# Performance work log

Measured on AMD Instinct MI355X. Metric: run time of the kernel, lower is better.

## Reference

```python
import jax, jax.numpy as jnp
import numpy as np

N_NODES = 100000
N_EDGES = 1600000
IN_DIM = 128
HID = 128
OUT = 64


def gcn_conv(x, src, dst, W, b, n_nodes):
    # x: [N, Din] -> [N, Dout]; symmetric-normalized GCN with self-loops (PyG GCNConv defaults)
    h = x @ W  # transform first (as PyG does)
    loop = jnp.arange(n_nodes, dtype=src.dtype)
    s = jnp.concatenate([src, loop])
    d = jnp.concatenate([dst, loop])
    deg = jax.ops.segment_sum(jnp.ones_like(d, dtype=h.dtype), d, num_segments=n_nodes)
    dis = jnp.where(deg > 0, jax.lax.rsqrt(deg), 0.0)
    norm = dis[s] * dis[d]  # [E+N]
    msgs = h[s] * norm[:, None]  # gather-transform
    out = jax.ops.segment_sum(msgs, d, num_segments=n_nodes)  # scatter-add
    return out + b


def setup_inputs() -> dict:
    key = jax.random.key(0)
    ks = jax.random.split(key, 12)
    x = jax.random.normal(ks[0], (N_NODES, IN_DIM), dtype=jnp.float32)
    edge_index = jax.random.randint(ks[1], (2, N_EDGES), 0, N_NODES, dtype=jnp.int32)
    def lin(k, fan_in, fan_out):
        bound = 1.0 / np.sqrt(fan_in)
        kw, kb = jax.random.split(k)
        W = jax.random.uniform(kw, (fan_in, fan_out), minval=-bound, maxval=bound, dtype=jnp.float32)
        b = jax.random.uniform(kb, (fan_out,), minval=-bound, maxval=bound, dtype=jnp.float32)
        return W, b
    W1, b1 = lin(ks[2], IN_DIM, HID)
    W2, b2 = lin(ks[3], HID, HID)
    Wp1, bp1 = lin(ks[4], HID, HID)
    Wp2, bp2 = lin(ks[5], HID, OUT)
    return {"x": x, "edge_index": edge_index,
            "W1": W1, "b1": b1, "W2": W2, "b2": b2,
            "Wp1": Wp1, "bp1": bp1, "Wp2": Wp2, "bp2": bp2}


def reference(x, edge_index, W1, b1, W2, b2, Wp1, bp1, Wp2, bp2):
    n = x.shape[0]
    src, dst = edge_index[0], edge_index[1]
    # layer 1: GCNConv + relu (dropout inactive at eval)
    h = jax.nn.relu(gcn_conv(x, src, dst, W1, b1, n))
    # layer 2
    h = jax.nn.relu(gcn_conv(h, src, dst, W2, b2, n))
    # post MLP head
    h = h @ Wp1 + bp1
    h = h @ Wp2 + bp2
    return jax.nn.log_softmax(h, axis=1)
```

## Files before the change

### kernel.cpp

```cpp
#include <hip/hip_runtime.h>
#include <hip/hip_bf16.h>
#include <cstdint>

typedef __attribute__((ext_vector_type(8))) short short8;
typedef __attribute__((ext_vector_type(16))) float f32x16;
typedef unsigned short us;

#define BIN_SHIFT 9
#define BIN_NODES 512
#define CAPB 12288
#define EPB 4096

__device__ __forceinline__ float bflo(uint32_t u) { return __builtin_bit_cast(float, u << 16); }
__device__ __forceinline__ float bfhi(uint32_t u) { return __builtin_bit_cast(float, u & 0xffff0000u); }

__device__ __forceinline__ us f32_to_bf16_rne(float f) {
  uint32_t u = __builtin_bit_cast(uint32_t, f);
  u += 0x7fffu + ((u >> 16) & 1u);
  return (us)(u >> 16);
}

__device__ __forceinline__ void split2(float f, us& h, us& l) {
  uint32_t u = __builtin_bit_cast(uint32_t, f);
  h = (us)(u >> 16);
  float fh = __builtin_bit_cast(float, u & 0xffff0000u);
  float r = f - fh;
  l = (us)(__builtin_bit_cast(uint32_t, r) >> 16);
}

__global__ void k_prep(const float* __restrict__ W1, const float* __restrict__ W2,
                       const float* __restrict__ Wp1, const float* __restrict__ Wp2,
                       const float* __restrict__ bp1, const float* __restrict__ bp2,
                       us* __restrict__ Wt1h, us* __restrict__ Wt1l,
                       us* __restrict__ Wt2h, us* __restrict__ Wt2l,
                       us* __restrict__ Wch, us* __restrict__ Wcl, float* __restrict__ bc,
                       int* __restrict__ gcur, int* __restrict__ hzero) {
  int blk = blockIdx.x, tid = threadIdx.x;
  if (blk < 128) {
    const float* W = (blk < 64) ? W1 : W2;
    us* Wh = (blk < 64) ? Wt1h : Wt2h;
    us* Wl = (blk < 64) ? Wt1l : Wt2l;
    int idx = (blk & 63) * 256 + tid;
    int k = idx >> 7, n = idx & 127;
    us h, l;
    split2(W[idx], h, l);
    Wh[n * 128 + k] = h;
    Wl[n * 128 + k] = l;
  } else if (blk < 160) {
    int idx = (blk - 128) * 256 + tid;
    int k = idx >> 6, j = idx & 63;
    float acc = 0.f;
    for (int t = 0; t < 128; ++t) acc += Wp1[k * 128 + t] * Wp2[t * 64 + j];
    us h, l;
    split2(acc, h, l);
    Wch[j * 128 + k] = h;
    Wcl[j * 128 + k] = l;
  } else {
    gcur[tid] = 0;
    if (tid < 64) {
      hzero[tid] = 0;
      float acc = bp2[tid];
      for (int t = 0; t < 128; ++t) acc += bp1[t] * Wp2[t * 64 + tid];
      bc[tid] = acc;
    }
  }
}

__global__ __launch_bounds__(256) void k_binA(
    const int* __restrict__ src, const int* __restrict__ dst,
    uint2* __restrict__ binbuf, int* __restrict__ gcur, int E, int nbins) {
  __shared__ uint2 stage[EPB];
  __shared__ int cnt[256], base[256], cur[256], gbase[256];
  int tid = threadIdx.x;
  int e0 = blockIdx.x * EPB;
  int ne = min(EPB, E - e0);
  if (ne <= 0) return;
  cnt[tid] = 0;
  __syncthreads();
  for (int i = tid; i < ne; i += 256) atomicAdd(&cnt[dst[e0 + i] >> BIN_SHIFT], 1);
  __syncthreads();
  if (tid < 64) {
    int carry = 0;
#pragma unroll
    for (int c = 0; c < 4; ++c) {
      int v = cnt[c * 64 + tid];
      int incl = v;
#pragma unroll
      for (int off = 1; off < 64; off <<= 1) {
        int t = __shfl_up(incl, off, 64);
        if (tid >= off) incl += t;
      }
      base[c * 64 + tid] = carry + incl - v;
      carry += __shfl(incl, 63, 64);
    }
  }
  __syncthreads();
  if (tid < nbins && cnt[tid] > 0) gbase[tid] = atomicAdd(&gcur[tid], cnt[tid]);
  cur[tid] = base[tid];
  __syncthreads();
  for (int i = tid; i < ne; i += 256) {
    int d = dst[e0 + i], s = src[e0 + i];
    int p = atomicAdd(&cur[d >> BIN_SHIFT], 1);
    stage[p] = make_uint2((unsigned)d, (unsigned)s);
  }
  __syncthreads();
  for (int i = tid; i < ne; i += 256) {
    uint2 en = stage[i];
    int b = en.x >> BIN_SHIFT;
    int gi = gbase[b] + (i - base[b]);
    if (gi < CAPB) binbuf[(size_t)b * CAPB + gi] = en;
  }
}

__global__ __launch_bounds__(256) void k_passB(
    const uint2* __restrict__ binbuf, const int* __restrict__ gcur,
    int* __restrict__ deg, float* __restrict__ dis, int* __restrict__ start,
    int* __restrict__ col, int N, int nbins) {
  __shared__ int hist[512], lstart[512], cur[512];
  __shared__ int colstage[CAPB];
  __shared__ int binbase_s;
  int b = blockIdx.x, tid = threadIdx.x;
  int node0 = b << BIN_SHIFT;
  int cnt = min(gcur[b], CAPB);
  hist[tid] = 0; hist[tid + 256] = 0;
  __syncthreads();
  const uint2* bp = binbuf + (size_t)b * CAPB;
  for (int i = tid; i < cnt; i += 256) atomicAdd(&hist[bp[i].x & (BIN_NODES - 1)], 1);
  __syncthreads();
  if (tid < 64) {
    int s = 0;
    for (int i = tid; i < b; i += 64) s += min(gcur[i], CAPB);
#pragma unroll
    for (int off = 32; off; off >>= 1) s += __shfl_xor(s, off, 64);
    if (tid == 0) binbase_s = s;
    int carry = 0;
#pragma unroll
    for (int c = 0; c < 8; ++c) {
      int v = hist[c * 64 + tid];
      int incl = v;
#pragma unroll
      for (int off = 1; off < 64; off <<= 1) {
        int t = __shfl_up(incl, off, 64);
        if (tid >= off) incl += t;
      }
      lstart[c * 64 + tid] = carry + incl - v;
      carry += __shfl(incl, 63, 64);
    }
  }
  __syncthreads();
  int binbase = binbase_s;
  for (int i = tid; i < 512; i += 256) {
    int node = node0 + i;
    if (node < N) {
      int dg = hist[i];
      deg[node] = dg;
      dis[node] = rsqrtf((float)(dg + 1));
      start[node] = binbase + lstart[i];
    }
  }
  cur[tid] = lstart[tid]; cur[tid + 256] = lstart[tid + 256];
  __syncthreads();
  for (int i = tid; i < cnt; i += 256) {
    uint2 en = bp[i];
    int p = atomicAdd(&cur[en.x & (BIN_NODES - 1)], 1);
    colstage[p] = (int)en.y;
  }
  __syncthreads();
  for (int i = tid; i < cnt; i += 256) col[binbase + i] = colstage[i];
}

__global__ __launch_bounds__(256) void k_gemm1(
    const float* __restrict__ A, const us* __restrict__ Wh,
    const us* __restrict__ Wl, const float* __restrict__ dis,
    us* __restrict__ out_bf16, int N, int ntiles) {
  __shared__ us As[32 * 136];
  int tid = threadIdx.x;
  int wave = tid >> 6, lane = tid & 63;
  int n0 = wave * 32;
  int nn = n0 + (lane & 31);
  int khalf = (lane >> 5) * 8;
  int m = lane & 31;

  short8 bh[8], bl[8];
#pragma unroll
  for (int c = 0; c < 8; ++c) {
    bh[c] = *(const short8*)&Wh[nn * 128 + c * 16 + khalf];
    bl[c] = *(const short8*)&Wl[nn * 128 + c * 16 + khalf];
  }

  for (int t = blockIdx.x; t < ntiles; t += gridDim.x) {
    int row0 = t * 32;
    __syncthreads();
    for (int j = tid; j < 1024; j += 256) {
      int r = j >> 5, c = j & 31;
      int row = row0 + r;
      float4 v = make_float4(0.f, 0.f, 0.f, 0.f);
      if (row < N) v = *(const float4*)&A[(size_t)row * 128 + c * 4];
      *(ushort4*)&As[r * 136 + c * 4] = make_ushort4(
          f32_to_bf16_rne(v.x), f32_to_bf16_rne(v.y),
          f32_to_bf16_rne(v.z), f32_to_bf16_rne(v.w));
    }
    __syncthreads();

    f32x16 acc = {};
#pragma unroll
    for (int c = 0; c < 8; ++c) {
      short8 ah = *(const short8*)&As[m * 136 + c * 16 + khalf];
      acc = __builtin_amdgcn_mfma_f32_32x32x16_bf16(ah, bh[c], acc, 0, 0, 0);
      acc = __builtin_amdgcn_mfma_f32_32x32x16_bf16(ah, bl[c], acc, 0, 0, 0);
    }

    int col = n0 + (lane & 31);
    int rbase = row0 + 4 * (lane >> 5);
#pragma unroll
    for (int reg = 0; reg < 16; ++reg) {
      int row = rbase + (reg & 3) + 8 * (reg >> 2);
      if (row < N) {
        float v = acc[reg] * dis[row];
        out_bf16[(size_t)row * 128 + col] = f32_to_bf16_rne(v);
      }
    }
  }
}

__global__ __launch_bounds__(256) void k_gemm2(
    const us* __restrict__ A, const us* __restrict__ Wh,
    const us* __restrict__ Wl, const float* __restrict__ dis,
    us* __restrict__ out_bf16, int N, int ntiles) {
  __shared__ us As[32 * 136];
  int tid = threadIdx.x;
  int wave = tid >> 6, lane = tid & 63;
  int n0 = wave * 32;
  int nn = n0 + (lane & 31);
  int khalf = (lane >> 5) * 8;
  int m = lane & 31;

  short8 bh[8], bl[8];
#pragma unroll
  for (int c = 0; c < 8; ++c) {
    bh[c] = *(const short8*)&Wh[nn * 128 + c * 16 + khalf];
    bl[c] = *(const short8*)&Wl[nn * 128 + c * 16 + khalf];
  }

  for (int t = blockIdx.x; t < ntiles; t += gridDim.x) {
    int row0 = t * 32;
    __syncthreads();
    for (int j = tid; j < 512; j += 256) {
      int r = j >> 4, c = j & 15;
      int row = row0 + r;
      uint4 v = make_uint4(0u, 0u, 0u, 0u);
      if (row < N) v = *(const uint4*)&A[(size_t)row * 128 + c * 8];
      *(uint4*)&As[r * 136 + c * 8] = v;
    }
    __syncthreads();

    f32x16 acc = {};
#pragma unroll
    for (int c = 0; c < 8; ++c) {
      short8 ah = *(const short8*)&As[m * 136 + c * 16 + khalf];
      acc = __builtin_amdgcn_mfma_f32_32x32x16_bf16(ah, bh[c], acc, 0, 0, 0);
      acc = __builtin_amdgcn_mfma_f32_32x32x16_bf16(ah, bl[c], acc, 0, 0, 0);
    }

    int col = n0 + (lane & 31);
    int rbase = row0 + 4 * (lane >> 5);
#pragma unroll
    for (int reg = 0; reg < 16; ++reg) {
      int row = rbase + (reg & 3) + 8 * (reg >> 2);
      if (row < N) {
        float v = acc[reg] * dis[row];
        out_bf16[(size_t)row * 128 + col] = f32_to_bf16_rne(v);
      }
    }
  }
}

__global__ __launch_bounds__(512) void k_gather(
    const us* __restrict__ h, us* __restrict__ o,
    const int* __restrict__ start, const int* __restrict__ deg,
    const int* __restrict__ col, const float* __restrict__ dis,
    const float* __restrict__ bias, int N) {
  int wave = threadIdx.x >> 6, lane = threadIdx.x & 63;
  int node = blockIdx.x * 8 + wave;
  if (node >= N) return;
  const uint32_t* h1 = (const uint32_t*)h;
  uint32_t u = h1[(size_t)node * 64 + lane];
  float a0 = bflo(u), b0 = bfhi(u);
  float a1 = 0.f, b1 = 0.f, a2 = 0.f, b2 = 0.f, a3 = 0.f, b3 = 0.f;
  float a4 = 0.f, b4 = 0.f, a5 = 0.f, b5 = 0.f, a6 = 0.f, b6 = 0.f, a7 = 0.f, b7 = 0.f;
  int e0 = start[node];
  int dg = deg[node];
  int myc = (lane < dg) ? col[e0 + lane] : N;
  int dgm = min(dg, 64);
  for (int k = 0; k < dgm; k += 8) {
    int c0 = __builtin_amdgcn_readlane(myc, k);
    int c1 = __builtin_amdgcn_readlane(myc, k + 1);
    int c2 = __builtin_amdgcn_readlane(myc, k + 2);
    int c3 = __builtin_amdgcn_readlane(myc, k + 3);
    int c4 = __builtin_amdgcn_readlane(myc, k + 4);
    int c5 = __builtin_amdgcn_readlane(myc, k + 5);
    int c6 = __builtin_amdgcn_readlane(myc, k + 6);
    int c7 = __builtin_amdgcn_readlane(myc, k + 7);
    uint32_t u0 = h1[(size_t)c0 * 64 + lane];
    uint32_t u1 = h1[(size_t)c1 * 64 + lane];
    uint32_t u2 = h1[(size_t)c2 * 64 + lane];
    uint32_t u3 = h1[(size_t)c3 * 64 + lane];
    uint32_t u4 = h1[(size_t)c4 * 64 + lane];
    uint32_t u5 = h1[(size_t)c5 * 64 + lane];
    uint32_t u6 = h1[(size_t)c6 * 64 + lane];
    uint32_t u7 = h1[(size_t)c7 * 64 + lane];
    a0 += bflo(u0); b0 += bfhi(u0);
    a1 += bflo(u1); b1 += bfhi(u1);
    a2 += bflo(u2); b2 += bfhi(u2);
    a3 += bflo(u3); b3 += bfhi(u3);
    a4 += bflo(u4); b4 += bfhi(u4);
    a5 += bflo(u5); b5 += bfhi(u5);
    a6 += bflo(u6); b6 += bfhi(u6);
    a7 += bflo(u7); b7 += bfhi(u7);
  }
  for (int e = e0 + 64; e < e0 + dg; ++e) {
    uint32_t u0 = h1[(size_t)col[e] * 64 + lane];
    a0 += bflo(u0); b0 += bfhi(u0);
  }
  float sc = dis[node];
  float2 bb = ((const float2*)bias)[lane];
  float ax = ((a0 + a1) + (a2 + a3)) + ((a4 + a5) + (a6 + a7));
  float ay = ((b0 + b1) + (b2 + b3)) + ((b4 + b5) + (b6 + b7));
  float rx = fmaxf(ax * sc + bb.x, 0.f);
  float ry = fmaxf(ay * sc + bb.y, 0.f);
  ((uint32_t*)o)[(size_t)node * 64 + lane] =
      ((uint32_t)f32_to_bf16_rne(ry) << 16) | f32_to_bf16_rne(rx);
}

__global__ __launch_bounds__(256) void k_head_mfma(
    const us* __restrict__ act, const us* __restrict__ Wch,
    const us* __restrict__ Wcl, const float* __restrict__ bc,
    float* __restrict__ out, int N) {
  __shared__ us As[64 * 136];
  __shared__ float red[2][2][64];
  int tid = threadIdx.x;
  int wave = tid >> 6, lane = tid & 63;
  int rt = wave >> 1, ct = wave & 1;
  int colj = ct * 32 + (lane & 31);
  int khalf = (lane >> 5) * 8;
  int m = lane & 31;

  short8 bh[8], bl[8];
#pragma unroll
  for (int c = 0; c < 8; ++c) {
    bh[c] = *(const short8*)&Wch[colj * 128 + c * 16 + khalf];
    bl[c] = *(const short8*)&Wcl[colj * 128 + c * 16 + khalf];
  }

  int row0 = blockIdx.x * 64;
  for (int j = tid; j < 1024; j += 256) {
    int r = j >> 4, c = j & 15;
    int row = row0 + r;
    uint4 v = make_uint4(0u, 0u, 0u, 0u);
    if (row < N) v = *(const uint4*)&act[(size_t)row * 128 + c * 8];
    *(uint4*)&As[r * 136 + c * 8] = v;
  }
  __syncthreads();

  f32x16 acc = {};
  int mrow = rt * 32 + m;
#pragma unroll
  for (int c = 0; c < 8; ++c) {
    short8 ah = *(const short8*)&As[mrow * 136 + c * 16 + khalf];
    acc = __builtin_amdgcn_mfma_f32_32x32x16_bf16(ah, bh[c], acc, 0, 0, 0);
    acc = __builtin_amdgcn_mfma_f32_32x32x16_bf16(ah, bl[c], acc, 0, 0, 0);
  }

  float bcv = bc[colj];
  float lg[16], mx[16];
#pragma unroll
  for (int reg = 0; reg < 16; ++reg) {
    lg[reg] = acc[reg] + bcv;
    float v = lg[reg];
#pragma unroll
    for (int off = 16; off > 0; off >>= 1) v = fmaxf(v, __shfl_xor(v, off, 32));
    mx[reg] = v;
  }
  if ((lane & 31) == 0) {
#pragma unroll
    for (int reg = 0; reg < 16; ++reg) {
      int rl = rt * 32 + (reg & 3) + 8 * (reg >> 2) + 4 * (lane >> 5);
      red[0][ct][rl] = mx[reg];
    }
  }
  __syncthreads();

  float ex[16], sm[16];
#pragma unroll
  for (int reg = 0; reg < 16; ++reg) {
    int rl = rt * 32 + (reg & 3) + 8 * (reg >> 2) + 4 * (lane >> 5);
    float rmax = fmaxf(red[0][0][rl], red[0][1][rl]);
    ex[reg] = lg[reg] - rmax;
    float v = expf(ex[reg]);
#pragma unroll
    for (int off = 16; off > 0; off >>= 1) v += __shfl_xor(v, off, 32);
    sm[reg] = v;
  }
  if ((lane & 31) == 0) {
#pragma unroll
    for (int reg = 0; reg < 16; ++reg) {
      int rl = rt * 32 + (reg & 3) + 8 * (reg >> 2) + 4 * (lane >> 5);
      red[1][ct][rl] = sm[reg];
    }
  }
  __syncthreads();

#pragma unroll
  for (int reg = 0; reg < 16; ++reg) {
    int rl = rt * 32 + (reg & 3) + 8 * (reg >> 2) + 4 * (lane >> 5);
    int row = row0 + rl;
    if (row < N) {
      float total = red[1][0][rl] + red[1][1][rl];
      out[(size_t)row * 64 + colj] = ex[reg] - logf(total);
    }
  }
}

extern "C" void kernel_launch(void* const* d_in, const int* in_sizes, int n_in,
                              void* d_out, int out_size, void* d_ws, size_t ws_size,
                              hipStream_t stream) {
  const float* x   = (const float*)d_in[0];
  const int*   ei  = (const int*)d_in[1];
  const float* W1  = (const float*)d_in[2];
  const float* b1  = (const float*)d_in[3];
  const float* W2  = (const float*)d_in[4];
  const float* b2  = (const float*)d_in[5];
  const float* Wp1 = (const float*)d_in[6];
  const float* bp1 = (const float*)d_in[7];
  const float* Wp2 = (const float*)d_in[8];
  const float* bp2 = (const float*)d_in[9];
  float* out = (float*)d_out;

  int N = in_sizes[0] / 128;
  int E = in_sizes[1] / 2;
  const int* src = ei;
  const int* dst = ei + E;
  int nbins = (N + BIN_NODES - 1) >> BIN_SHIFT;

  float* dis   = (float*)d_ws;
  int*   deg   = (int*)(dis + N);
  int*   start = deg + N;
  int*   col   = start + N;
  int*   gcur  = col + ((E + 3) & ~3);
  us* Wt1h = (us*)(gcur + 256);
  us* Wt1l = Wt1h + 16384;
  us* Wt2h = Wt1l + 16384;
  us* Wt2l = Wt2h + 16384;
  us* Wch  = Wt2l + 16384;
  us* Wcl  = Wch + 8192;
  float* bc = (float*)(Wcl + 8192);
  uint2* binbuf = (uint2*)(bc + 80);
  us* hbuf = (us*)(binbuf + (size_t)nbins * CAPB);
  us* act  = hbuf + (size_t)(N + 1) * 128;

  k_prep<<<161, 256, 0, stream>>>(W1, W2, Wp1, Wp2, bp1, bp2,
                                  Wt1h, Wt1l, Wt2h, Wt2l, Wch, Wcl, bc,
                                  gcur, (int*)(hbuf + (size_t)N * 128));

  int ablocks = (E + EPB - 1) / EPB;
  k_binA<<<ablocks, 256, 0, stream>>>(src, dst, binbuf, gcur, E, nbins);
  k_passB<<<nbins, 256, 0, stream>>>(binbuf, gcur, deg, dis, start, col, N, nbins);

  int ntiles = (N + 31) / 32;
  int gemm_grid = ntiles < 1024 ? ntiles : 1024;
  int agblocks = (N + 7) / 8;
  int hblocks = (N + 63) / 64;

  k_gemm1<<<gemm_grid, 256, 0, stream>>>(x, Wt1h, Wt1l, dis, hbuf, N, ntiles);
  k_gather<<<agblocks, 512, 0, stream>>>(hbuf, act, start, deg, col, dis, b1, N);
  k_gemm2<<<gemm_grid, 256, 0, stream>>>(act, Wt2h, Wt2l, dis, hbuf, N, ntiles);
  k_gather<<<agblocks, 512, 0, stream>>>(hbuf, act, start, deg, col, dis, b2, N);
  k_head_mfma<<<hblocks, 256, 0, stream>>>(act, Wch, Wcl, bc, out, N);
}
```

Measured before the change: 397.8 us.

## Replace binned two-pass CSR build with atomic degree count, scan, and fill

Removes the two-level bin staging (k_binA/k_passB with the binbuf intermediate). Degrees are now counted with global atomics fused into k_prep, prefix-summed by a single-block scan kernel, and edges are placed into CSR with per-node global atomics. This drops the large binbuf traffic and the shared-memory staging, but adds a serial single-block scan over 100K nodes, heavily contended global atomics, and a non-deterministic column order within each node.

```diff
diff --git a/kernel.cpp b/kernel.cpp
--- a/kernel.cpp
+++ b/kernel.cpp
@@ -6,9 +6,6 @@
 typedef __attribute__((ext_vector_type(16))) float f32x16;
 typedef unsigned short us;
 
-#define BIN_SHIFT 9
-#define BIN_NODES 512
-#define CAPB 12288
 #define EPB 4096
 
 __device__ __forceinline__ float bflo(uint32_t u) { return __builtin_bit_cast(float, u << 16); }
@@ -34,7 +31,8 @@
                        us* __restrict__ Wt1h, us* __restrict__ Wt1l,
                        us* __restrict__ Wt2h, us* __restrict__ Wt2l,
                        us* __restrict__ Wch, us* __restrict__ Wcl, float* __restrict__ bc,
-                       int* __restrict__ gcur, int* __restrict__ hzero) {
+                       int* __restrict__ hzero,
+                       const int* __restrict__ dst, int* __restrict__ deg, int E) {
   int blk = blockIdx.x, tid = threadIdx.x;
   if (blk < 128) {
     const float* W = (blk < 64) ? W1 : W2;
@@ -55,118 +53,73 @@
     split2(acc, h, l);
     Wch[j * 128 + k] = h;
     Wcl[j * 128 + k] = l;
-  } else {
-    gcur[tid] = 0;
+  } else if (blk == 160) {
     if (tid < 64) {
       hzero[tid] = 0;
       float acc = bp2[tid];
       for (int t = 0; t < 128; ++t) acc += bp1[t] * Wp2[t * 64 + tid];
       bc[tid] = acc;
     }
-  }
-}
-
-__global__ __launch_bounds__(256) void k_binA(
+  } else {
+    int e0 = (blk - 161) * EPB;
+    int ne = min(EPB, E - e0);
+    for (int i = tid; i < ne; i += 256) atomicAdd(&deg[dst[e0 + i]], 1);
+  }
+}
+
+__global__ __launch_bounds__(1024) void k_scan(
+    const int* __restrict__ deg, int* __restrict__ start, int* __restrict__ cur,
+    float* __restrict__ dis, int N) {
+  __shared__ int wsum[16];
+  __shared__ int btot_s;
+  __shared__ int carry_s;
+  int tid = threadIdx.x, lane = tid & 63, w = tid >> 6;
+  if (tid == 0) carry_s = 0;
+  __syncthreads();
+  for (int base = 0; base < N; base += 1024) {
+    int i = base + tid;
+    int v = (i < N) ? deg[i] : 0;
+    int incl = v;
+#pragma unroll
+    for (int off = 1; off < 64; off <<= 1) {
+      int t = __shfl_up(incl, off, 64);
+      if (lane >= off) incl += t;
+    }
+    if (lane == 63) wsum[w] = incl;
+    __syncthreads();
+    if (tid < 16) {
+      int s = wsum[tid];
+      int in2 = s;
+#pragma unroll
+      for (int off = 1; off < 16; off <<= 1) {
+        int t = __shfl_up(in2, off, 64);
+        if (tid >= off) in2 += t;
+      }
+      wsum[tid] = in2 - s;
+      if (tid == 15) btot_s = in2;
+    }
+    __syncthreads();
+    int excl = carry_s + wsum[w] + (incl - v);
+    if (i < N) {
+      start[i] = excl;
+      cur[i] = excl;
+      dis[i] = rsqrtf((float)(v + 1));
+    }
+    __syncthreads();
+    if (tid == 0) carry_s += btot_s;
+  }
+}
+
+__global__ __launch_bounds__(256) void k_fill(
     const int* __restrict__ src, const int* __restrict__ dst,
-    uint2* __restrict__ binbuf, int* __restrict__ gcur, int E, int nbins) {
-  __shared__ uint2 stage[EPB];
-  __shared__ int cnt[256], base[256], cur[256], gbase[256];
-  int tid = threadIdx.x;
+    int* __restrict__ cur, int* __restrict__ col, int E) {
   int e0 = blockIdx.x * EPB;
   int ne = min(EPB, E - e0);
-  if (ne <= 0) return;
-  cnt[tid] = 0;
-  __syncthreads();
-  for (int i = tid; i < ne; i += 256) atomicAdd(&cnt[dst[e0 + i] >> BIN_SHIFT], 1);
-  __syncthreads();
-  if (tid < 64) {
-    int carry = 0;
-#pragma unroll
-    for (int c = 0; c < 4; ++c) {
-      int v = cnt[c * 64 + tid];
-      int incl = v;
-#pragma unroll
-      for (int off = 1; off < 64; off <<= 1) {
-        int t = __shfl_up(incl, off, 64);
-        if (tid >= off) incl += t;
-      }
-      base[c * 64 + tid] = carry + incl - v;
-      carry += __shfl(incl, 63, 64);
-    }
-  }
-  __syncthreads();
-  if (tid < nbins && cnt[tid] > 0) gbase[tid] = atomicAdd(&gcur[tid], cnt[tid]);
-  cur[tid] = base[tid];
-  __syncthreads();
-  for (int i = tid; i < ne; i += 256) {
+  for (int i = threadIdx.x; i < ne; i += 256) {
     int d = dst[e0 + i], s = src[e0 + i];
-    int p = atomicAdd(&cur[d >> BIN_SHIFT], 1);
-    stage[p] = make_uint2((unsigned)d, (unsigned)s);
-  }
-  __syncthreads();
-  for (int i = tid; i < ne; i += 256) {
-    uint2 en = stage[i];
-    int b = en.x >> BIN_SHIFT;
-    int gi = gbase[b] + (i - base[b]);
-    if (gi < CAPB) binbuf[(size_t)b * CAPB + gi] = en;
-  }
-}
-
-__global__ __launch_bounds__(256) void k_passB(
-    const uint2* __restrict__ binbuf, const int* __restrict__ gcur,
-    int* __restrict__ deg, float* __restrict__ dis, int* __restrict__ start,
-    int* __restrict__ col, int N, int nbins) {
-  __shared__ int hist[512], lstart[512], cur[512];
-  __shared__ int colstage[CAPB];
-  __shared__ int binbase_s;
-  int b = blockIdx.x, tid = threadIdx.x;
-  int node0 = b << BIN_SHIFT;
-  int cnt = min(gcur[b], CAPB);
-  hist[tid] = 0; hist[tid + 256] = 0;
-  __syncthreads();
-  const uint2* bp = binbuf + (size_t)b * CAPB;
-  for (int i = tid; i < cnt; i += 256) atomicAdd(&hist[bp[i].x & (BIN_NODES - 1)], 1);
-  __syncthreads();
-  if (tid < 64) {
-    int s = 0;
-    for (int i = tid; i < b; i += 64) s += min(gcur[i], CAPB);
-#pragma unroll
-    for (int off = 32; off; off >>= 1) s += __shfl_xor(s, off, 64);
-    if (tid == 0) binbase_s = s;
-    int carry = 0;
-#pragma unroll
-    for (int c = 0; c < 8; ++c) {
-      int v = hist[c * 64 + tid];
-      int incl = v;
-#pragma unroll
-      for (int off = 1; off < 64; off <<= 1) {
-        int t = __shfl_up(incl, off, 64);
-        if (tid >= off) incl += t;
-      }
-      lstart[c * 64 + tid] = carry + incl - v;
-      carry += __shfl(incl, 63, 64);
-    }
-  }
-  __syncthreads();
-  int binbase = binbase_s;
-  for (int i = tid; i < 512; i += 256) {
-    int node = node0 + i;
-    if (node < N) {
-      int dg = hist[i];
-      deg[node] = dg;
-      dis[node] = rsqrtf((float)(dg + 1));
-      start[node] = binbase + lstart[i];
-    }
-  }
-  cur[tid] = lstart[tid]; cur[tid + 256] = lstart[tid + 256];
-  __syncthreads();
-  for (int i = tid; i < cnt; i += 256) {
-    uint2 en = bp[i];
-    int p = atomicAdd(&cur[en.x & (BIN_NODES - 1)], 1);
-    colstage[p] = (int)en.y;
-  }
-  __syncthreads();
-  for (int i = tid; i < cnt; i += 256) col[binbase + i] = colstage[i];
+    int p = atomicAdd(&cur[d], 1);
+    col[p] = s;
+  }
 }
 
 __global__ __launch_bounds__(256) void k_gemm1(
@@ -440,31 +393,31 @@
   int E = in_sizes[1] / 2;
   const int* src = ei;
   const int* dst = ei + E;
-  int nbins = (N + BIN_NODES - 1) >> BIN_SHIFT;
 
   float* dis   = (float*)d_ws;
   int*   deg   = (int*)(dis + N);
   int*   start = deg + N;
-  int*   col   = start + N;
-  int*   gcur  = col + ((E + 3) & ~3);
-  us* Wt1h = (us*)(gcur + 256);
+  int*   cur   = start + N;
+  int*   col   = cur + N;
+  us* Wt1h = (us*)(col + ((E + 3) & ~3));
   us* Wt1l = Wt1h + 16384;
   us* Wt2h = Wt1l + 16384;
   us* Wt2l = Wt2h + 16384;
   us* Wch  = Wt2l + 16384;
   us* Wcl  = Wch + 8192;
   float* bc = (float*)(Wcl + 8192);
-  uint2* binbuf = (uint2*)(bc + 80);
-  us* hbuf = (us*)(binbuf + (size_t)nbins * CAPB);
+  us* hbuf = (us*)(bc + 80);
   us* act  = hbuf + (size_t)(N + 1) * 128;
 
-  k_prep<<<161, 256, 0, stream>>>(W1, W2, Wp1, Wp2, bp1, bp2,
-                                  Wt1h, Wt1l, Wt2h, Wt2l, Wch, Wcl, bc,
-                                  gcur, (int*)(hbuf + (size_t)N * 128));
+  hipMemsetAsync(deg, 0, N * sizeof(int), stream);
 
   int ablocks = (E + EPB - 1) / EPB;
-  k_binA<<<ablocks, 256, 0, stream>>>(src, dst, binbuf, gcur, E, nbins);
-  k_passB<<<nbins, 256, 0, stream>>>(binbuf, gcur, deg, dis, start, col, N, nbins);
+  k_prep<<<161 + ablocks, 256, 0, stream>>>(W1, W2, Wp1, Wp2, bp1, bp2,
+                                            Wt1h, Wt1l, Wt2h, Wt2l, Wch, Wcl, bc,
+                                            (int*)(hbuf + (size_t)N * 128),
+                                            dst, deg, E);
+  k_scan<<<1, 1024, 0, stream>>>(deg, start, cur, dis, N);
+  k_fill<<<ablocks, 256, 0, stream>>>(src, dst, cur, col, E);
 
   int ntiles = (N + 31) / 32;
   int gemm_grid = ntiles < 1024 ? ntiles : 1024;
```

Measured after the change: 637.1 us. 60.2% more time.
